# Performance work log

Hardware: AMD Instinct MI355X
Metric: run time of the kernel (lower is better)

The kernel has to match this reference:

```python
import jax, jax.numpy as jnp
import numpy as np

IMG_H, IMG_W = 800, 1344
STRIDE = 16
FH, FW = IMG_H // STRIDE, IMG_W // STRIDE  # 50, 84
C = 1024
N_PROP = 3000
K_KEEP = 512          # post-NMS proposals kept by merge_proposals
POOL = 14             # C4 ROI-align output resolution
NMS_THRESH = 0.7
NUM_CLASSES = 80


def _make_boxes(key, n):
    r = jax.random.uniform(key, (n, 4))
    cx = r[:, 0] * IMG_W
    cy = r[:, 1] * IMG_H
    w = 16.0 + r[:, 2] * 480.0
    h = 16.0 + r[:, 3] * 480.0
    x0 = jnp.clip(cx - w / 2, 0.0, IMG_W)
    y0 = jnp.clip(cy - h / 2, 0.0, IMG_H)
    x1 = jnp.clip(cx + w / 2, 0.0, IMG_W)
    y1 = jnp.clip(cy + h / 2, 0.0, IMG_H)
    return jnp.stack([x0, y0, x1, y1], axis=-1)


def setup_inputs() -> dict:
    key = jax.random.key(0)
    ks = jax.random.split(key, 14)
    feat = jax.random.normal(ks[0], (C, FH, FW), jnp.float32)
    boxes1 = _make_boxes(ks[1], N_PROP)
    boxes2 = _make_boxes(ks[2], N_PROP)
    logits1 = jax.random.normal(ks[3], (N_PROP,), jnp.float32)
    logits2 = jax.random.normal(ks[4], (N_PROP,), jnp.float32)
    levels1 = jnp.zeros((N_PROP,), jnp.int32)  # single C4 level
    levels2 = jnp.zeros((N_PROP,), jnp.int32)
    scale1 = 1.0 + 0.02 * jax.random.normal(ks[5], (C,), jnp.float32)
    bias1 = 0.02 * jax.random.normal(ks[6], (C,), jnp.float32)
    scale2 = 1.0 + 0.02 * jax.random.normal(ks[7], (C,), jnp.float32)
    bias2 = 0.02 * jax.random.normal(ks[8], (C,), jnp.float32)
    W_cls1 = 0.01 * jax.random.normal(ks[9], (C, NUM_CLASSES + 1), jnp.float32)
    b_cls1 = jnp.zeros((NUM_CLASSES + 1,), jnp.float32)
    W_box1 = 0.001 * jax.random.normal(ks[10], (C, NUM_CLASSES * 4), jnp.float32)
    b_box1 = jnp.zeros((NUM_CLASSES * 4,), jnp.float32)
    W_cls2 = 0.01 * jax.random.normal(ks[11], (C, NUM_CLASSES + 1), jnp.float32)
    b_cls2 = jnp.zeros((NUM_CLASSES + 1,), jnp.float32)
    W_box2 = 0.001 * jax.random.normal(ks[12], (C, NUM_CLASSES * 4), jnp.float32)
    b_box2 = jnp.zeros((NUM_CLASSES * 4,), jnp.float32)
    return dict(feat=feat, boxes1=boxes1, boxes2=boxes2, logits1=logits1,
                logits2=logits2, levels1=levels1, levels2=levels2,
                scale1=scale1, bias1=bias1, scale2=scale2, bias2=bias2,
                W_cls1=W_cls1, b_cls1=b_cls1, W_box1=W_box1, b_box1=b_box1,
                W_cls2=W_cls2, b_cls2=b_cls2, W_box2=W_box2, b_box2=b_box2)


def _clip_boxes(boxes):
    return jnp.stack([jnp.clip(boxes[:, 0], 0.0, IMG_W),
                      jnp.clip(boxes[:, 1], 0.0, IMG_H),
                      jnp.clip(boxes[:, 2], 0.0, IMG_W),
                      jnp.clip(boxes[:, 3], 0.0, IMG_H)], axis=-1)


def _nms(boxes, scores, k, thresh):
    """Greedy NMS; returns k kept indices (fixed-size, jit-friendly)."""
    areas = (boxes[:, 2] - boxes[:, 0]) * (boxes[:, 3] - boxes[:, 1])

    def body(i, state):
        sw, keep = state
        idx = jnp.argmax(sw)
        keep = keep.at[i].set(idx.astype(jnp.int32))
        b = boxes[idx]
        ix0 = jnp.maximum(b[0], boxes[:, 0])
        iy0 = jnp.maximum(b[1], boxes[:, 1])
        ix1 = jnp.minimum(b[2], boxes[:, 2])
        iy1 = jnp.minimum(b[3], boxes[:, 3])
        inter = jnp.maximum(ix1 - ix0, 0.0) * jnp.maximum(iy1 - iy0, 0.0)
        iou = inter / (areas[idx] + areas - inter + 1e-9)
        sw = jnp.where(iou > thresh, -jnp.inf, sw)
        sw = sw.at[idx].set(-jnp.inf)
        return sw, keep

    keep0 = jnp.zeros((k,), jnp.int32)
    _, keep = jax.lax.fori_loop(0, k, body, (scores, keep0))
    return keep


def _roi_align(feat, boxes, spatial_scale, pool):
    """ROIAlign (aligned=True, sampling_ratio=1). feat [C,H,W], boxes [R,4] -> [R,C,pool,pool]."""
    Cc, H, W = feat.shape
    b = boxes * spatial_scale - 0.5
    x0, y0, x1, y1 = b[:, 0], b[:, 1], b[:, 2], b[:, 3]
    bw = (x1 - x0) / pool
    bh = (y1 - y0) / pool
    grid = jnp.arange(pool, dtype=feat.dtype) + 0.5
    xs = x0[:, None] + grid[None, :] * bw[:, None]  # [R,P]
    ys = y0[:, None] + grid[None, :] * bh[:, None]  # [R,P]
    yf = jnp.floor(ys); xf = jnp.floor(xs)
    ly = ys - yf; lx = xs - xf
    y0c = jnp.clip(yf.astype(jnp.int32), 0, H - 1)
    y1c = jnp.clip(yf.astype(jnp.int32) + 1, 0, H - 1)
    x0c = jnp.clip(xf.astype(jnp.int32), 0, W - 1)
    x1c = jnp.clip(xf.astype(jnp.int32) + 1, 0, W - 1)

    def g(Y, X):  # gather -> [C,R,P,P]
        return feat[:, Y[:, :, None], X[:, None, :]]

    wy0 = (1.0 - ly); wy1 = ly  # [R,P]
    wx0 = (1.0 - lx); wx1 = lx
    out = (g(y0c, x0c) * (wy0[:, :, None] * wx0[:, None, :])
           + g(y0c, x1c) * (wy0[:, :, None] * wx1[:, None, :])
           + g(y1c, x0c) * (wy1[:, :, None] * wx0[:, None, :])
           + g(y1c, x1c) * (wy1[:, :, None] * wx1[:, None, :]))
    return jnp.transpose(out, (1, 0, 2, 3))  # [R,C,P,P]


def _box_head(roi_feats, scale, bias, W_cls, b_cls, W_box, b_box):
    bf = roi_feats * scale[None, :, None, None] + bias[None, :, None, None]
    x = bf.mean(axis=(2, 3))  # [R,C]
    return bf, x @ W_cls + b_cls, x @ W_box + b_box


def reference(feat, boxes1, boxes2, logits1, logits2, levels1, levels2,
              scale1, bias1, scale2, bias2,
              W_cls1, b_cls1, W_box1, b_box1,
              W_cls2, b_cls2, W_box2, b_box2):
    boxes = _clip_boxes(jnp.concatenate([boxes1, boxes2], axis=0))
    scores = jnp.concatenate([logits1, logits2], axis=0)
    levels = jnp.concatenate([levels1, levels2], axis=0)
    # batched_nms level-offset trick (all zeros for single C4 level)
    off = levels.astype(boxes.dtype)[:, None] * float(max(IMG_H, IMG_W) + 1)
    keep = _nms(boxes + off, scores, K_KEEP, NMS_THRESH)
    prop = boxes[keep]  # [K,4] merged proposals

    roi = _roi_align(feat, prop, 1.0 / STRIDE, POOL)  # [K,C,P,P]
    bf1, s1, d1 = _box_head(roi, scale1, bias1, W_cls1, b_cls1, W_box1, b_box1)
    bf2, s2, d2 = _box_head(roi, scale2, bias2, W_cls2, b_cls2, W_box2, b_box2)
    return (bf1, bf2, s1, s2, d1, prop, feat)
```

## Files before the change

kernel.cpp:

```cpp
#include <hip/hip_runtime.h>

#define FHH 50
#define FWW 84
#define HW 4200
#define NBOX 6000
#define NPAD 6144
#define KKEEP 512
#define WSTRIDE 192

typedef float f32x2 __attribute__((ext_vector_type(2)));
typedef float f32x4v __attribute__((ext_vector_type(4)));
typedef _Float16 f16x4 __attribute__((ext_vector_type(4)));
typedef _Float16 f16x2 __attribute__((ext_vector_type(2)));

#define OFF_BF1  0ULL
#define OFF_BF2  102760448ULL
#define OFF_S1   205520896ULL
#define OFF_S2   205562368ULL
#define OFF_D1   205603840ULL
#define OFF_PROP 205767680ULL
#define OFF_FEAT 205769728ULL

__global__ __launch_bounds__(256) void k_transpose(const float* __restrict__ feat,
                                                   _Float16* __restrict__ featH,
                                                   float* __restrict__ out_feat) {
  __shared__ float t[32][33];
  int hw0 = blockIdx.x * 32;
  int c0  = blockIdx.y * 32;
  int tx = threadIdx.x & 31, ty = threadIdx.x >> 5;
#pragma unroll
  for (int p = 0; p < 4; ++p) {
    int c = c0 + ty + p * 8;
    int hw = hw0 + tx;
    if (hw < HW) {
      float v = feat[(size_t)c * HW + hw];
      t[ty + p * 8][tx] = v;
      __builtin_nontemporal_store(v, &out_feat[(size_t)c * HW + hw]);
    }
  }
  __syncthreads();
#pragma unroll
  for (int p = 0; p < 4; ++p) {
    int hw = hw0 + ty + p * 8;
    int c = c0 + tx;
    if (hw < HW) featH[((size_t)hw << 10) + c] = (_Float16)t[tx][ty + p * 8];
  }
}

__global__ __launch_bounds__(256) void k_prep(const float4* __restrict__ boxes1,
                                              const float4* __restrict__ boxes2,
                                              const float* __restrict__ logits1,
                                              const float* __restrict__ logits2,
                                              const int* __restrict__ levels1,
                                              const int* __restrict__ levels2,
                                              float4* __restrict__ nbox,
                                              float* __restrict__ area,
                                              unsigned long long* __restrict__ keys,
                                              int* __restrict__ rank) {
  int i = blockIdx.x * 256 + threadIdx.x;
  if (i >= NPAD) return;
  if (i >= NBOX) { keys[i] = 0ULL; return; }
  rank[i] = 0;
  float4 b; float sc; int lv;
  if (i < 3000) { b = boxes1[i]; sc = logits1[i]; lv = levels1[i]; }
  else          { b = boxes2[i - 3000]; sc = logits2[i - 3000]; lv = levels2[i - 3000]; }
  float x0 = fminf(fmaxf(b.x, 0.f), 1344.f);
  float y0 = fminf(fmaxf(b.y, 0.f), 800.f);
  float x1 = fminf(fmaxf(b.z, 0.f), 1344.f);
  float y1 = fminf(fmaxf(b.w, 0.f), 800.f);
  float off = __fmul_rn((float)lv, 1345.0f);
  x0 = __fadd_rn(x0, off); y0 = __fadd_rn(y0, off);
  x1 = __fadd_rn(x1, off); y1 = __fadd_rn(y1, off);
  nbox[i] = make_float4(x0, y0, x1, y1);
  area[i] = __fmul_rn(__fsub_rn(x1, x0), __fsub_rn(y1, y0));
  unsigned u = __float_as_uint(sc);
  u = (u & 0x80000000u) ? ~u : (u | 0x80000000u);
  keys[i] = ((unsigned long long)u << 32) | (unsigned)(0xFFFFFFFFu - (unsigned)i);
}

__global__ __launch_bounds__(256) void k_rank(const unsigned long long* __restrict__ keys,
                                              int* __restrict__ rank) {
  __shared__ unsigned long long ks[1024];
  int jb = blockIdx.y;
  for (int t = threadIdx.x; t < 1024; t += 256) ks[t] = keys[jb * 1024 + t];
  __syncthreads();
  int i = blockIdx.x * 256 + threadIdx.x;
  if (i >= NBOX) return;
  unsigned long long ki = keys[i];
  int c = 0;
  for (int j = 0; j < 1024; ++j) c += (ks[j] > ki) ? 1 : 0;
  if (c) atomicAdd(&rank[i], c);
}

__global__ __launch_bounds__(256) void k_scatter(const float4* __restrict__ nbox,
                                                 const float* __restrict__ area,
                                                 const int* __restrict__ rank,
                                                 float4* __restrict__ sboxes,
                                                 float* __restrict__ sarea,
                                                 int* __restrict__ sorig) {
  int i = blockIdx.x * 256 + threadIdx.x;
  if (i >= NBOX) return;
  int r = rank[i];
  sboxes[r] = nbox[i];
  sarea[r] = area[i];
  sorig[r] = i;
}

__global__ __launch_bounds__(192) void k_mask(const float4* __restrict__ sboxes,
                                              const float* __restrict__ sarea,
                                              unsigned* __restrict__ mask) {
  int i0 = blockIdx.x * 4;
  int w = threadIdx.x;
  float4 b0 = sboxes[i0 + 0], b1 = sboxes[i0 + 1], b2 = sboxes[i0 + 2], b3 = sboxes[i0 + 3];
  float a0 = sarea[i0 + 0], a1 = sarea[i0 + 1], a2 = sarea[i0 + 2], a3 = sarea[i0 + 3];
  unsigned m0 = 0, m1 = 0, m2 = 0, m3 = 0;
  int jbase = w * 32;
  for (int bb = 0; bb < 32; ++bb) {
    int j = jbase + bb;
    if (j >= NBOX) break;
    float4 bj = sboxes[j];
    float aj = sarea[j];
#define IOU_BIT(BR, AR, MR)                                                          \
    {                                                                                \
      float ix0 = fmaxf(BR.x, bj.x), iy0 = fmaxf(BR.y, bj.y);                        \
      float ix1 = fminf(BR.z, bj.z), iy1 = fminf(BR.w, bj.w);                        \
      float iw = fmaxf(__fsub_rn(ix1, ix0), 0.f), ih = fmaxf(__fsub_rn(iy1, iy0), 0.f); \
      float inter = __fmul_rn(iw, ih);                                               \
      float den = __fadd_rn(__fsub_rn(__fadd_rn(AR, aj), inter), 1e-9f);             \
      float iou = __fdiv_rn(inter, den);                                             \
      if (iou > 0.7f) MR |= (1u << bb);                                              \
    }
    IOU_BIT(b0, a0, m0) IOU_BIT(b1, a1, m1) IOU_BIT(b2, a2, m2) IOU_BIT(b3, a3, m3)
#undef IOU_BIT
  }
  mask[(size_t)(i0 + 0) * WSTRIDE + w] = m0;
  mask[(size_t)(i0 + 1) * WSTRIDE + w] = m1;
  mask[(size_t)(i0 + 2) * WSTRIDE + w] = m2;
  mask[(size_t)(i0 + 3) * WSTRIDE + w] = m3;
}

#define SCAN_CH 64
__global__ __launch_bounds__(256) void k_scan(const unsigned* __restrict__ mask,
                                              const int* __restrict__ sorig,
                                              int* __restrict__ keep) {
  __shared__ unsigned srows[2][SCAN_CH * WSTRIDE];
  __shared__ int s_sorig[2][SCAN_CH];
  __shared__ int s_done, s_kept;
  int tid = threadIdx.x;
  if (tid == 0) { s_done = 0; s_kept = 0; }
  for (int idx = tid; idx < SCAN_CH * WSTRIDE; idx += 256) srows[0][idx] = mask[idx];
  if (tid < SCAN_CH) s_sorig[0][tid] = sorig[tid];
  __syncthreads();
  unsigned r0 = 0, r1 = 0, r2 = 0;
  int lane = tid;
  int kept = 0;
  for (int g = 0; g < 94; ++g) {
    int cur = g & 1, nxt = cur ^ 1;
    if (tid >= 64) {
      int gn = g + 1;
      if (gn < 94) {
        size_t gbase = (size_t)gn * SCAN_CH * WSTRIDE;
        for (int idx = tid - 64; idx < SCAN_CH * WSTRIDE; idx += 192) {
          size_t gi = gbase + idx;
          srows[nxt][idx] = (gi < (size_t)NBOX * WSTRIDE) ? mask[gi] : 0u;
        }
        if (tid - 64 < SCAN_CH) {
          int i2 = gn * SCAN_CH + (tid - 64);
          s_sorig[nxt][tid - 64] = (i2 < NBOX) ? sorig[i2] : 0;
        }
      }
    } else {
      int base = g * SCAN_CH;
      int nrows = min(SCAN_CH, NBOX - base);
      const unsigned* sb = srows[cur];
      unsigned p0 = sb[lane], p1 = sb[64 + lane], p2 = sb[128 + lane];
      for (int rr = 0; rr < nrows; ++rr) {
        unsigned c0v = p0, c1v = p1, c2v = p2;
        int rn = (rr + 1 < nrows) ? rr + 1 : rr;
        p0 = sb[rn * WSTRIDE + lane];
        p1 = sb[rn * WSTRIDE + 64 + lane];
        p2 = sb[rn * WSTRIDE + 128 + lane];
        int i = base + rr;
        int w = i >> 5, b = i & 31;
        int wl = w & 63, wc = w >> 6;
        unsigned rsel = (wc == 0) ? r0 : ((wc == 1) ? r1 : r2);
        unsigned rw = __shfl(rsel, wl);
        if (!((rw >> b) & 1u)) {
          r0 |= c0v; r1 |= c1v; r2 |= c2v;
          if (lane == 0) keep[kept] = s_sorig[cur][rr];
          kept++;
          if (kept >= KKEEP) break;
        }
      }
      if (lane == 0) { s_kept = kept; if (kept >= KKEEP) s_done = 1; }
    }
    __syncthreads();
    if (s_done) break;
  }
  __syncthreads();
  int fk = s_kept;
  for (int k = fk + tid; k < KKEEP; k += 256) keep[k] = 0;
}

__global__ __launch_bounds__(256) void k_bilin(const int* __restrict__ keep,
                                               const float4* __restrict__ boxes1,
                                               const float4* __restrict__ boxes2,
                                               float4* __restrict__ prop,
                                               float4* __restrict__ bilinW,
                                               int4* __restrict__ bilinA) {
  int r = blockIdx.x;
  __shared__ float4 spb;
  if (threadIdx.x == 0) {
    int o = keep[r];
    float4 b = (o < 3000) ? boxes1[o] : boxes2[o - 3000];
    float4 p = make_float4(fminf(fmaxf(b.x, 0.f), 1344.f),
                           fminf(fmaxf(b.y, 0.f), 800.f),
                           fminf(fmaxf(b.z, 0.f), 1344.f),
                           fminf(fmaxf(b.w, 0.f), 800.f));
    prop[r] = p;
    spb = p;
  }
  __syncthreads();
  int bin = threadIdx.x;
  if (bin >= 196) return;
  float4 pb = spb;
  const float ss = 0.0625f;
  float x0s = pb.x * ss - 0.5f, y0s = pb.y * ss - 0.5f;
  float bw = (pb.z * ss - 0.5f - x0s) / 14.0f;
  float bh = (pb.w * ss - 0.5f - y0s) / 14.0f;
  int py = bin / 14, px = bin - py * 14;
  float xs = x0s + ((float)px + 0.5f) * bw;
  float ys = y0s + ((float)py + 0.5f) * bh;
  float xf = floorf(xs), yf = floorf(ys);
  float lx = xs - xf, ly = ys - yf;
  int ix = (int)xf, iy = (int)yf;
  int x0c = min(max(ix, 0), FWW - 1), x1c = min(max(ix + 1, 0), FWW - 1);
  int y0c = min(max(iy, 0), FHH - 1), y1c = min(max(iy + 1, 0), FHH - 1);
  float wy0 = 1.f - ly, wx0 = 1.f - lx;
  bilinW[r * 196 + bin] = make_float4(wy0 * wx0, wy0 * lx, ly * wx0, ly * lx);
  bilinA[r * 196 + bin] = make_int4((y0c * FWW + x0c) << 10, (y0c * FWW + x1c) << 10,
                                    (y1c * FWW + x0c) << 10, (y1c * FWW + x1c) << 10);
}

__global__ __launch_bounds__(256) void k_roi(const _Float16* __restrict__ featH,
                                             const float4* __restrict__ bilinW,
                                             const int4* __restrict__ bilinA,
                                             const float* __restrict__ scale1,
                                             const float* __restrict__ bias1,
                                             const float* __restrict__ scale2,
                                             const float* __restrict__ bias2,
                                             float* __restrict__ bf1,
                                             float* __restrict__ bf2,
                                             float* __restrict__ x1w,
                                             float* __restrict__ x2w) {
  __shared__ _Float16 tile[32 * 200];
  __shared__ float part2f[4 * 32];
  __shared__ float sc1[32], bi1[32], sc2[32], bi2[32];
  int bid = blockIdx.x;
  int r = bid & 511;
  int c0 = (bid >> 9) * 32;
  int tid = threadIdx.x;
  int l8 = tid & 7, bg = tid >> 3;
  if (tid < 32) {
    sc1[tid] = scale1[c0 + tid]; bi1[tid] = bias1[c0 + tid];
    sc2[tid] = scale2[c0 + tid]; bi2[tid] = bias2[c0 + tid];
  }
  const _Float16* fTb = featH + c0 + l8 * 4;
  const float4* bW = bilinW + r * 196;
  const int4* bA = bilinA + r * 196;
  float4 acc = make_float4(0.f, 0.f, 0.f, 0.f);

#define ROI_BODY(BB)                                                              \
  {                                                                               \
    float4 w = bW[BB]; int4 a = bA[BB];                                           \
    f16x4 g00 = *(const f16x4*)(fTb + a.x);                                       \
    f16x4 g01 = *(const f16x4*)(fTb + a.y);                                       \
    f16x4 g10 = *(const f16x4*)(fTb + a.z);                                       \
    f16x4 g11 = *(const f16x4*)(fTb + a.w);                                       \
    float vx = (float)g00.x * w.x + (float)g01.x * w.y + (float)g10.x * w.z + (float)g11.x * w.w; \
    float vy = (float)g00.y * w.x + (float)g01.y * w.y + (float)g10.y * w.z + (float)g11.y * w.w; \
    float vz = (float)g00.z * w.x + (float)g01.z * w.y + (float)g10.z * w.z + (float)g11.z * w.w; \
    float vw = (float)g00.w * w.x + (float)g01.w * w.y + (float)g10.w * w.z + (float)g11.w * w.w; \
    acc.x += vx; acc.y += vy; acc.z += vz; acc.w += vw;                           \
    int tb = l8 * 800 + (BB);                                                     \
    tile[tb] = (_Float16)vx; tile[tb + 200] = (_Float16)vy;                       \
    tile[tb + 400] = (_Float16)vz; tile[tb + 600] = (_Float16)vw;                 \
  }

  int bb = bg;
#pragma unroll
  for (int i = 0; i < 6; ++i, bb += 32) ROI_BODY(bb)
  if (bg < 4) ROI_BODY(192 + bg)
#undef ROI_BODY

  acc.x += __shfl_xor(acc.x, 8);  acc.y += __shfl_xor(acc.y, 8);
  acc.z += __shfl_xor(acc.z, 8);  acc.w += __shfl_xor(acc.w, 8);
  acc.x += __shfl_xor(acc.x, 16); acc.y += __shfl_xor(acc.y, 16);
  acc.z += __shfl_xor(acc.z, 16); acc.w += __shfl_xor(acc.w, 16);
  acc.x += __shfl_xor(acc.x, 32); acc.y += __shfl_xor(acc.y, 32);
  acc.z += __shfl_xor(acc.z, 32); acc.w += __shfl_xor(acc.w, 32);
  if ((tid & 63) < 8) {
    int wv = tid >> 6;
    part2f[wv * 32 + l8 * 4 + 0] = acc.x;
    part2f[wv * 32 + l8 * 4 + 1] = acc.y;
    part2f[wv * 32 + l8 * 4 + 2] = acc.z;
    part2f[wv * 32 + l8 * 4 + 3] = acc.w;
  }
  __syncthreads();
  if (tid < 32) {
    float m = ((part2f[tid] + part2f[32 + tid]) + part2f[64 + tid]) + part2f[96 + tid];
    m = m / 196.0f;
    x1w[((size_t)r << 10) + c0 + tid] = m * sc1[tid] + bi1[tid];
    x2w[((size_t)r << 10) + c0 + tid] = m * sc2[tid] + bi2[tid];
  }
  size_t ob = ((size_t)((r << 10) + c0)) * 196;
  float* b1p = bf1 + ob;
  float* b2p = bf2 + ob;
  for (int it = 0; it < 7; ++it) {
    int q = tid + it * 256;
    if (q < 1568) {
      int cl = q / 49;
      int pos = (q - cl * 49) * 4;
      f16x4 h = *(const f16x4*)&tile[cl * 200 + pos];
      float v0 = (float)h.x, v1 = (float)h.y, v2 = (float)h.z, v3 = (float)h.w;
      float s1v = sc1[cl], b1v = bi1[cl], s2v = sc2[cl], b2v = bi2[cl];
      f32x4v o1 = { v0 * s1v + b1v, v1 * s1v + b1v, v2 * s1v + b1v, v3 * s1v + b1v };
      f32x4v o2 = { v0 * s2v + b2v, v1 * s2v + b2v, v2 * s2v + b2v, v3 * s2v + b2v };
      *(f32x4v*)(b1p + 4 * q) = o1;
      *(f32x4v*)(b2p + 4 * q) = o2;
    }
  }
}

__global__ __launch_bounds__(256) void k_gemm(const float* __restrict__ x1,
                                              const float* __restrict__ x2,
                                              const float* __restrict__ Wc1, const float* __restrict__ bc1,
                                              const float* __restrict__ Wb1, const float* __restrict__ bb1,
                                              const float* __restrict__ Wc2, const float* __restrict__ bc2,
                                              float* __restrict__ s1, float* __restrict__ d1,
                                              float* __restrict__ s2) {
  int z = blockIdx.z;
  const float* A; const float* W; const float* bias; float* out; int N;
  if (z == 0)      { A = x1; W = Wc1; bias = bc1; out = s1; N = 81; }
  else if (z == 1) { A = x1; W = Wb1; bias = bb1; out = d1; N = 320; }
  else             { A = x2; W = Wc2; bias = bc2; out = s2; N = 81; }
  int n0 = blockIdx.y * 32;
  if (n0 >= N) return;
  int m0 = blockIdx.x * 32;
  __shared__ float As[32][34];
  __shared__ float Bs[32][34];
  int tid = threadIdx.x;
  int tx = tid & 15, ty = tid >> 4;
  float acc00 = 0, acc01 = 0, acc10 = 0, acc11 = 0;
  for (int k0 = 0; k0 < 1024; k0 += 32) {
    int mm = tid >> 3, g = tid & 7;
    float4 av = *(const float4*)(A + (size_t)(m0 + mm) * 1024 + k0 + g * 4);
    As[g * 4 + 0][mm] = av.x; As[g * 4 + 1][mm] = av.y;
    As[g * 4 + 2][mm] = av.z; As[g * 4 + 3][mm] = av.w;
    int nn = tid & 31, kh = tid >> 5;
#pragma unroll
    for (int qq = 0; qq < 4; ++qq) {
      int kk = kh + 8 * qq;
      int n = n0 + nn;
      Bs[kk][nn] = (n < N) ? W[(size_t)(k0 + kk) * N + n] : 0.f;
    }
    __syncthreads();
#pragma unroll
    for (int kk = 0; kk < 32; ++kk) {
      float2 a = *(const float2*)&As[kk][2 * ty];
      float2 b = *(const float2*)&Bs[kk][2 * tx];
      acc00 += a.x * b.x; acc01 += a.x * b.y;
      acc10 += a.y * b.x; acc11 += a.y * b.y;
    }
    __syncthreads();
  }
  int m = m0 + 2 * ty, n = n0 + 2 * tx;
  if (n < N) {
    out[(size_t)m * N + n] = acc00 + bias[n];
    out[(size_t)(m + 1) * N + n] = acc10 + bias[n];
  }
  if (n + 1 < N) {
    out[(size_t)m * N + n + 1] = acc01 + bias[n + 1];
    out[(size_t)(m + 1) * N + n + 1] = acc11 + bias[n + 1];
  }
}

extern "C" void kernel_launch(void* const* d_in, const int* in_sizes, int n_in,
                              void* d_out, int out_size, void* d_ws, size_t ws_size,
                              hipStream_t stream) {
  (void)in_sizes; (void)n_in; (void)out_size; (void)ws_size;
  const float* feat    = (const float*)d_in[0];
  const float4* boxes1 = (const float4*)d_in[1];
  const float4* boxes2 = (const float4*)d_in[2];
  const float* logits1 = (const float*)d_in[3];
  const float* logits2 = (const float*)d_in[4];
  const int* levels1   = (const int*)d_in[5];
  const int* levels2   = (const int*)d_in[6];
  const float* scale1  = (const float*)d_in[7];
  const float* bias1   = (const float*)d_in[8];
  const float* scale2  = (const float*)d_in[9];
  const float* bias2   = (const float*)d_in[10];
  const float* W_cls1  = (const float*)d_in[11];
  const float* b_cls1  = (const float*)d_in[12];
  const float* W_box1  = (const float*)d_in[13];
  const float* b_box1  = (const float*)d_in[14];
  const float* W_cls2  = (const float*)d_in[15];
  const float* b_cls2  = (const float*)d_in[16];

  float* out = (float*)d_out;
  char* w = (char*)d_ws;
  _Float16* featH           = (_Float16*)(w + 0);
  unsigned long long* keys  = (unsigned long long*)(w + 17203200);
  float4* nbox              = (float4*)(w + 17252352);
  float* area               = (float*)(w + 17348352);
  int* rank                 = (int*)(w + 17372352);
  float4* sboxes            = (float4*)(w + 17396352);
  float* sarea              = (float*)(w + 17492352);
  int* sorig                = (int*)(w + 17516352);
  unsigned* mask            = (unsigned*)(w + 17540352);
  int* keep                 = (int*)(w + 22148352);
  float* x1w                = (float*)(w + 22150400);
  float* x2w                = (float*)(w + 24247552);
  float4* bilinW            = (float4*)(w + 17540352);
  int4* bilinA              = (int4*)(w + 19145984);

  k_transpose<<<dim3(132, 32), 256, 0, stream>>>(feat, featH, out + OFF_FEAT);
  k_prep<<<24, 256, 0, stream>>>(boxes1, boxes2, logits1, logits2, levels1, levels2,
                                 nbox, area, keys, rank);
  k_rank<<<dim3(24, 6), 256, 0, stream>>>(keys, rank);
  k_scatter<<<24, 256, 0, stream>>>(nbox, area, rank, sboxes, sarea, sorig);
  k_mask<<<1500, 192, 0, stream>>>(sboxes, sarea, mask);
  k_scan<<<1, 256, 0, stream>>>(mask, sorig, keep);
  k_bilin<<<512, 256, 0, stream>>>(keep, boxes1, boxes2,
                                   (float4*)(out + OFF_PROP), bilinW, bilinA);
  k_roi<<<16384, 256, 0, stream>>>(featH, bilinW, bilinA,
                                   scale1, bias1, scale2, bias2,
                                   out + OFF_BF1, out + OFF_BF2, x1w, x2w);
  k_gemm<<<dim3(16, 10, 3), 256, 0, stream>>>(x1w, x2w, W_cls1, b_cls1, W_box1, b_box1,
                                              W_cls2, b_cls2,
                                              out + OFF_S1, out + OFF_D1, out + OFF_S2);
}
```

Before: 492.7 us.

## Widen ROI-align channel tile to 64 with 16-byte gathers and nontemporal stores

The ROI-align kernel now handles 64 channels per block instead of 32, so each thread gathers 8 fp16 channels per bilinear corner with 16-byte loads. This halves the grid and the number of times each block reloads the bilinear weight and address tables. The shared tile is stored bin-major with a padded stride, and the output pass reads it transposed with scalar LDS loads. Outputs are written with nontemporal stores to keep the 400MB bf1/bf2 streams out of cache, at the cost of more register and LDS use per block.

```diff
diff --git a/kernel.cpp b/kernel.cpp
--- a/kernel.cpp
+++ b/kernel.cpp
@@ -10,6 +10,7 @@
 
 typedef float f32x2 __attribute__((ext_vector_type(2)));
 typedef float f32x4v __attribute__((ext_vector_type(4)));
+typedef _Float16 f16x8 __attribute__((ext_vector_type(8)));
 typedef _Float16 f16x4 __attribute__((ext_vector_type(4)));
 typedef _Float16 f16x2 __attribute__((ext_vector_type(2)));
 
@@ -253,38 +254,40 @@
                                              float* __restrict__ bf2,
                                              float* __restrict__ x1w,
                                              float* __restrict__ x2w) {
-  __shared__ _Float16 tile[32 * 200];
-  __shared__ float part2f[4 * 32];
-  __shared__ float sc1[32], bi1[32], sc2[32], bi2[32];
+  __shared__ _Float16 tile[196 * 72];
+  __shared__ float part2f[4 * 64];
+  __shared__ float sc1[64], bi1[64], sc2[64], bi2[64];
   int bid = blockIdx.x;
   int r = bid & 511;
-  int c0 = (bid >> 9) * 32;
+  int c0 = (bid >> 9) * 64;
   int tid = threadIdx.x;
   int l8 = tid & 7, bg = tid >> 3;
-  if (tid < 32) {
+  if (tid < 64) {
     sc1[tid] = scale1[c0 + tid]; bi1[tid] = bias1[c0 + tid];
     sc2[tid] = scale2[c0 + tid]; bi2[tid] = bias2[c0 + tid];
   }
-  const _Float16* fTb = featH + c0 + l8 * 4;
+  const _Float16* fTb = featH + c0 + l8 * 8;
   const float4* bW = bilinW + r * 196;
   const int4* bA = bilinA + r * 196;
-  float4 acc = make_float4(0.f, 0.f, 0.f, 0.f);
+  float acc[8];
+#pragma unroll
+  for (int j = 0; j < 8; ++j) acc[j] = 0.f;
 
 #define ROI_BODY(BB)                                                              \
   {                                                                               \
     float4 w = bW[BB]; int4 a = bA[BB];                                           \
-    f16x4 g00 = *(const f16x4*)(fTb + a.x);                                       \
-    f16x4 g01 = *(const f16x4*)(fTb + a.y);                                       \
-    f16x4 g10 = *(const f16x4*)(fTb + a.z);                                       \
-    f16x4 g11 = *(const f16x4*)(fTb + a.w);                                       \
-    float vx = (float)g00.x * w.x + (float)g01.x * w.y + (float)g10.x * w.z + (float)g11.x * w.w; \
-    float vy = (float)g00.y * w.x + (float)g01.y * w.y + (float)g10.y * w.z + (float)g11.y * w.w; \
-    float vz = (float)g00.z * w.x + (float)g01.z * w.y + (float)g10.z * w.z + (float)g11.z * w.w; \
-    float vw = (float)g00.w * w.x + (float)g01.w * w.y + (float)g10.w * w.z + (float)g11.w * w.w; \
-    acc.x += vx; acc.y += vy; acc.z += vz; acc.w += vw;                           \
-    int tb = l8 * 800 + (BB);                                                     \
-    tile[tb] = (_Float16)vx; tile[tb + 200] = (_Float16)vy;                       \
-    tile[tb + 400] = (_Float16)vz; tile[tb + 600] = (_Float16)vw;                 \
+    f16x8 g00 = *(const f16x8*)(fTb + a.x);                                       \
+    f16x8 g01 = *(const f16x8*)(fTb + a.y);                                       \
+    f16x8 g10 = *(const f16x8*)(fTb + a.z);                                       \
+    f16x8 g11 = *(const f16x8*)(fTb + a.w);                                       \
+    f16x8 vv;                                                                     \
+    _Pragma("unroll")                                                             \
+    for (int j = 0; j < 8; ++j) {                                                 \
+      float v = (float)g00[j] * w.x + (float)g01[j] * w.y                         \
+              + (float)g10[j] * w.z + (float)g11[j] * w.w;                        \
+      acc[j] += v; vv[j] = (_Float16)v;                                           \
+    }                                                                             \
+    *(f16x8*)(&tile[(BB) * 72 + l8 * 8]) = vv;                                    \
   }
 
   int bb = bg;
@@ -293,22 +296,20 @@
   if (bg < 4) ROI_BODY(192 + bg)
 #undef ROI_BODY
 
-  acc.x += __shfl_xor(acc.x, 8);  acc.y += __shfl_xor(acc.y, 8);
-  acc.z += __shfl_xor(acc.z, 8);  acc.w += __shfl_xor(acc.w, 8);
-  acc.x += __shfl_xor(acc.x, 16); acc.y += __shfl_xor(acc.y, 16);
-  acc.z += __shfl_xor(acc.z, 16); acc.w += __shfl_xor(acc.w, 16);
-  acc.x += __shfl_xor(acc.x, 32); acc.y += __shfl_xor(acc.y, 32);
-  acc.z += __shfl_xor(acc.z, 32); acc.w += __shfl_xor(acc.w, 32);
+#pragma unroll
+  for (int j = 0; j < 8; ++j) {
+    acc[j] += __shfl_xor(acc[j], 8);
+    acc[j] += __shfl_xor(acc[j], 16);
+    acc[j] += __shfl_xor(acc[j], 32);
+  }
   if ((tid & 63) < 8) {
     int wv = tid >> 6;
-    part2f[wv * 32 + l8 * 4 + 0] = acc.x;
-    part2f[wv * 32 + l8 * 4 + 1] = acc.y;
-    part2f[wv * 32 + l8 * 4 + 2] = acc.z;
-    part2f[wv * 32 + l8 * 4 + 3] = acc.w;
-  }
-  __syncthreads();
-  if (tid < 32) {
-    float m = ((part2f[tid] + part2f[32 + tid]) + part2f[64 + tid]) + part2f[96 + tid];
+#pragma unroll
+    for (int j = 0; j < 8; ++j) part2f[wv * 64 + l8 * 8 + j] = acc[j];
+  }
+  __syncthreads();
+  if (tid < 64) {
+    float m = ((part2f[tid] + part2f[64 + tid]) + part2f[128 + tid]) + part2f[192 + tid];
     m = m / 196.0f;
     x1w[((size_t)r << 10) + c0 + tid] = m * sc1[tid] + bi1[tid];
     x2w[((size_t)r << 10) + c0 + tid] = m * sc2[tid] + bi2[tid];
@@ -316,18 +317,20 @@
   size_t ob = ((size_t)((r << 10) + c0)) * 196;
   float* b1p = bf1 + ob;
   float* b2p = bf2 + ob;
-  for (int it = 0; it < 7; ++it) {
+  for (int it = 0; it < 13; ++it) {
     int q = tid + it * 256;
-    if (q < 1568) {
+    if (q < 3136) {
       int cl = q / 49;
       int pos = (q - cl * 49) * 4;
-      f16x4 h = *(const f16x4*)&tile[cl * 200 + pos];
-      float v0 = (float)h.x, v1 = (float)h.y, v2 = (float)h.z, v3 = (float)h.w;
+      float v0 = (float)tile[(pos + 0) * 72 + cl];
+      float v1 = (float)tile[(pos + 1) * 72 + cl];
+      float v2 = (float)tile[(pos + 2) * 72 + cl];
+      float v3 = (float)tile[(pos + 3) * 72 + cl];
       float s1v = sc1[cl], b1v = bi1[cl], s2v = sc2[cl], b2v = bi2[cl];
       f32x4v o1 = { v0 * s1v + b1v, v1 * s1v + b1v, v2 * s1v + b1v, v3 * s1v + b1v };
       f32x4v o2 = { v0 * s2v + b2v, v1 * s2v + b2v, v2 * s2v + b2v, v3 * s2v + b2v };
-      *(f32x4v*)(b1p + 4 * q) = o1;
-      *(f32x4v*)(b2p + 4 * q) = o2;
+      __builtin_nontemporal_store(o1, (f32x4v*)(b1p + 4 * q));
+      __builtin_nontemporal_store(o2, (f32x4v*)(b2p + 4 * q));
     }
   }
 }
@@ -433,9 +436,9 @@
   k_scan<<<1, 256, 0, stream>>>(mask, sorig, keep);
   k_bilin<<<512, 256, 0, stream>>>(keep, boxes1, boxes2,
                                    (float4*)(out + OFF_PROP), bilinW, bilinA);
-  k_roi<<<16384, 256, 0, stream>>>(featH, bilinW, bilinA,
-                                   scale1, bias1, scale2, bias2,
-                                   out + OFF_BF1, out + OFF_BF2, x1w, x2w);
+  k_roi<<<8192, 256, 0, stream>>>(featH, bilinW, bilinA,
+                                  scale1, bias1, scale2, bias2,
+                                  out + OFF_BF1, out + OFF_BF2, x1w, x2w);
   k_gemm<<<dim3(16, 10, 3), 256, 0, stream>>>(x1w, x2w, W_cls1, b_cls1, W_box1, b_box1,
                                               W_cls2, b_cls2,
                                               out + OFF_S1, out + OFF_D1, out + OFF_S2);
```

Measured after the change: 471.4 us. -4.3%, faster.
